# Kernel tuning notes

Hardware: AMD Instinct MI355X
Metric: run time of the kernel (lower is better)

Reference implementation:

```python
import jax, jax.numpy as jnp
import numpy as np

D_MODEL = 1024
D_INNER = 2048
D_STATE = 16
DT_RANK = 64
D_CONV = 4
EPS = 1e-5
B_SZ, L = 2, 2048


def setup_inputs() -> dict:
    key = jax.random.key(0)
    ks = jax.random.split(key, 8)
    s = 0.02
    inp = {
        "x": jax.random.normal(ks[0], (B_SZ, L, D_MODEL), jnp.float32),
        "in_proj_w": jax.random.normal(ks[1], (D_MODEL, 2 * D_INNER), jnp.float32) * s,
        "conv_w": jax.random.normal(ks[2], (D_INNER, 1, D_CONV), jnp.float32) * s,
        "conv_b": jnp.zeros((D_INNER,), jnp.float32),
        "x_proj_w": jax.random.normal(ks[3], (D_INNER, DT_RANK + 2 * D_STATE), jnp.float32) * s,
        "dt_proj_w": jax.random.normal(ks[4], (DT_RANK, D_INNER), jnp.float32) * s,
        "dt_proj_b": jax.random.normal(ks[5], (D_INNER,), jnp.float32) * s,
        "A_log": jnp.log(jnp.broadcast_to(jnp.arange(1, D_STATE + 1, dtype=jnp.float32), (D_INNER, D_STATE))),
        "D": jnp.ones((D_INNER,), jnp.float32),
        "out_proj_w": jax.random.normal(ks[6], (D_INNER, D_MODEL), jnp.float32) * s,
        "norm_w": jnp.ones((D_MODEL,), jnp.float32),
    }
    return inp


def _silu(x):
    return x * jax.nn.sigmoid(x)


def reference(x, in_proj_w, conv_w, conv_b, x_proj_w, dt_proj_w, dt_proj_b,
              A_log, D, out_proj_w, norm_w):
    b, l, d = x.shape
    # RMSNorm
    xn = x * jax.lax.rsqrt(jnp.mean(x * x, axis=-1, keepdims=True) + EPS) * norm_w
    # in_proj -> split into x branch and residual (gate) branch
    x_and_res = xn @ in_proj_w                      # (b, l, 2*d_inner)
    xi, res = jnp.split(x_and_res, 2, axis=-1)
    # causal depthwise conv1d (pad left d_conv-1, equivalent to torch pad+truncate)
    xc = jax.lax.conv_general_dilated(
        xi.transpose(0, 2, 1),                      # (b, d_inner, l)
        conv_w,                                     # (d_inner, 1, d_conv) = OIH
        window_strides=(1,),
        padding=[(D_CONV - 1, 0)],
        feature_group_count=D_INNER,
        dimension_numbers=("NCH", "OIH", "NCH"),
    ) + conv_b[None, :, None]
    xi = _silu(xc.transpose(0, 2, 1))               # (b, l, d_inner)
    # SSM parameters
    x_dbl = xi @ x_proj_w                           # (b, l, dt_rank + 2n)
    delta, Bm, Cm = jnp.split(x_dbl, [DT_RANK, DT_RANK + D_STATE], axis=-1)
    delta = jax.nn.softplus(delta @ dt_proj_w + dt_proj_b)   # (b, l, d_inner)
    A = -jnp.exp(A_log)                             # (d_inner, n)
    # discretize
    deltaA = jnp.exp(delta[..., None] * A)                          # (b,l,d,n)
    deltaB_u = delta[..., None] * Bm[:, :, None, :] * xi[..., None]  # (b,l,d,n)
    # selective scan over sequence length via lax.scan
    def step(state, inputs):
        dA_t, dBu_t, C_t = inputs                   # (b,d,n),(b,d,n),(b,n)
        state = dA_t * state + dBu_t
        y_t = jnp.einsum("bdn,bn->bd", state, C_t)
        return state, y_t
    state0 = jnp.zeros((b, D_INNER, D_STATE), xi.dtype)
    _, ys = jax.lax.scan(
        step, state0,
        (deltaA.transpose(1, 0, 2, 3), deltaB_u.transpose(1, 0, 2, 3), Cm.transpose(1, 0, 2)),
    )                                               # ys: (l, b, d_inner)
    y = ys.transpose(1, 0, 2) + xi * D              # skip connection D*u
    y = y * _silu(res)                              # gate
    out = y @ out_proj_w + x                        # out_proj + residual add
    return out
```

## Files before the change

kernel.cpp:

```cpp
#include <hip/hip_runtime.h>
#include <cstdint>

#define D_MODEL 1024
#define D_INNER 2048
#define NSTATE  16
#define DT_RANK 64
#define SEQ     2048
#define NBATCH  2
#define NTOK    (NBATCH * SEQ)

#define NC      32
#define CHK     64
#define NGRP    8

typedef float  f32x4  __attribute__((ext_vector_type(4)));
typedef __bf16 bf16x8 __attribute__((ext_vector_type(8)));
typedef short  s16x8  __attribute__((ext_vector_type(8)));

__device__ __forceinline__ unsigned short f2bf(float f) {
  union { float f; uint32_t u; } a; a.f = f;
  uint32_t u = a.u;
  uint32_t r = (u + 0x7FFFu + ((u >> 16) & 1u)) >> 16;
  return (unsigned short)r;
}
__device__ __forceinline__ float bf2f(unsigned short h) {
  union { uint32_t u; float f; } a; a.u = ((uint32_t)h) << 16;
  return a.f;
}

__device__ __forceinline__ void gload16(const void* g, void* l) {
  __builtin_amdgcn_global_load_lds((__attribute__((address_space(1))) void*)g,
                                   (__attribute__((address_space(3))) void*)l,
                                   16, 0, 0);
}

__device__ __forceinline__ void rms_body(const float* __restrict__ x, const float* __restrict__ nw,
                                         unsigned short* __restrict__ xn, int row, float* red) {
  const float4 v = ((const float4*)(x + (size_t)row * D_MODEL))[threadIdx.x];
  float ss = v.x*v.x + v.y*v.y + v.z*v.z + v.w*v.w;
  #pragma unroll
  for (int m = 32; m; m >>= 1) ss += __shfl_xor(ss, m);
  if ((threadIdx.x & 63) == 0) red[threadIdx.x >> 6] = ss;
  __syncthreads();
  const float tot = red[0] + red[1] + red[2] + red[3];
  const float rs = rsqrtf(tot * (1.0f / D_MODEL) + 1e-5f);
  const float4 w = ((const float4*)nw)[threadIdx.x];
  ushort4 o;
  o.x = f2bf(v.x * rs * w.x);
  o.y = f2bf(v.y * rs * w.y);
  o.z = f2bf(v.z * rs * w.z);
  o.w = f2bf(v.w * rs * w.w);
  ((ushort4*)(xn + (size_t)row * D_MODEL))[threadIdx.x] = o;
}

__device__ __forceinline__ void tr_body(const float* __restrict__ W, unsigned short* __restrict__ Wt,
                                        int K, int N, int Npad, int bx, int by, float (*tile)[33]) {
  const int tx = threadIdx.x & 31, ty = threadIdx.x >> 5;
  const int kt = by * 32, nt = bx * 32;
  #pragma unroll
  for (int i = 0; i < 4; ++i) {
    const int k = kt + ty + i*8, n = nt + tx;
    tile[ty + i*8][tx] = (k < K && n < N) ? W[(size_t)k * N + n] : 0.0f;
  }
  __syncthreads();
  #pragma unroll
  for (int i = 0; i < 4; ++i) {
    const int n = nt + ty + i*8, k = kt + tx;
    if (n < Npad && k < K) Wt[(size_t)n * K + k] = f2bf(tile[tx][ty + i*8]);
  }
}

__global__ __launch_bounds__(256) void prep_fused_kernel(const float* x, const float* nw, unsigned short* xn,
                                                         const float* W1, unsigned short* W1t,
                                                         const float* W2, unsigned short* W2t,
                                                         const float* W3, unsigned short* W3t,
                                                         const float* W4, unsigned short* W4t) {
  __shared__ float shbuf[32][33];
  const int b = blockIdx.x;
  if (b < 4096) {
    rms_body(x, nw, xn, b, &shbuf[0][0]);
  } else if (b < 8192) {
    const int i = b - 4096;
    tr_body(W1, W1t, 1024, 4096, 4096, i & 127, i >> 7, shbuf);
  } else if (b < 8448) {
    const int i = b - 8192;
    tr_body(W2, W2t, 2048, 96, 128, i & 3, i >> 2, shbuf);
  } else if (b < 8576) {
    const int i = b - 8448;
    tr_body(W3, W3t, 64, 2048, 2048, i & 63, i >> 6, shbuf);
  } else {
    const int i = b - 8576;
    tr_body(W4, W4t, 2048, 1024, 1024, i & 31, i >> 5, shbuf);
  }
}

__global__ __launch_bounds__(512, 2) void g0_inproj_kernel(const unsigned short* __restrict__ A,
                                                           const unsigned short* __restrict__ Bt,
                                                           unsigned short* __restrict__ xiOut,
                                                           unsigned short* __restrict__ resOut) {
  constexpr int K  = 1024;
  constexpr int NT = K / 64;
  __shared__ __align__(16) unsigned short sA[2][256 * 64];
  __shared__ __align__(16) unsigned short sB[2][256 * 64];
  const int tid = threadIdx.x;
  const int wid = tid >> 6, lane = tid & 63;
  const int wm = wid >> 2, wn = wid & 3;
  const int lr = lane & 15, kq = lane >> 4;
  const int m0 = blockIdx.y * 256, n0 = blockIdx.x * 256;

  f32x4 acc[8][4] = {};

  const int srow = tid >> 3;
  const int scol = 8 * ((tid & 7) ^ ((tid >> 3) & 7));
  const unsigned short* gA = A  + (size_t)(m0 + srow) * K + scol;
  const unsigned short* gB = Bt + (size_t)(n0 + srow) * K + scol;

  const int xsw = (lr & 7) << 4;
  const int cofs0 = ((kq * 16) ^ xsw) >> 1;
  const int cofs1 = ((64 + kq * 16) ^ xsw) >> 1;
  const int aRow = (wm * 128 + lr) * 64;
  const int bRow = (wn * 64 + lr) * 64;

  auto stage2 = [&](int p, int kt, int q) {
    const int k0 = kt * 64;
    gload16(gA + (size_t)q * 64 * K + k0, (char*)sA[p] + q * 8192 + tid * 16);
    gload16(gB + (size_t)q * 64 * K + k0, (char*)sB[p] + q * 8192 + tid * 16);
  };

  #pragma unroll
  for (int q = 0; q < 4; ++q) stage2(0, 0, q);
  __syncthreads();

  int p = 0;
  for (int kt = 0; kt < NT; ++kt) {
    const unsigned short* SA = sA[p];
    const unsigned short* SB = sB[p];
    bf16x8 b[4][2];
    #pragma unroll
    for (int q = 0; q < 4; ++q) {
      bf16x8 a[2][2];
      #pragma unroll
      for (int mi = 0; mi < 2; ++mi) {
        a[mi][0] = __builtin_bit_cast(bf16x8, *(const s16x8*)(SA + aRow + (2*q + mi) * 1024 + cofs0));
        a[mi][1] = __builtin_bit_cast(bf16x8, *(const s16x8*)(SA + aRow + (2*q + mi) * 1024 + cofs1));
      }
      if (q == 0) {
        #pragma unroll
        for (int nf = 0; nf < 4; ++nf) {
          b[nf][0] = __builtin_bit_cast(bf16x8, *(const s16x8*)(SB + bRow + nf * 1024 + cofs0));
          b[nf][1] = __builtin_bit_cast(bf16x8, *(const s16x8*)(SB + bRow + nf * 1024 + cofs1));
        }
      }
      if (kt + 1 < NT) stage2(p ^ 1, kt + 1, q);
      __builtin_amdgcn_s_barrier();
      __builtin_amdgcn_s_setprio(1);
      #pragma unroll
      for (int ks = 0; ks < 2; ++ks)
        #pragma unroll
        for (int mi = 0; mi < 2; ++mi)
          #pragma unroll
          for (int nf = 0; nf < 4; ++nf)
            acc[2*q + mi][nf] = __builtin_amdgcn_mfma_f32_16x16x32_bf16(a[mi][ks], b[nf][ks], acc[2*q + mi][nf], 0, 0, 0);
      __builtin_amdgcn_s_setprio(0);
      __builtin_amdgcn_s_barrier();
    }
    __syncthreads();
    p ^= 1;
  }

  #pragma unroll
  for (int mf = 0; mf < 8; ++mf) {
    #pragma unroll
    for (int nf = 0; nf < 4; ++nf) {
      const int col = n0 + wn * 64 + nf * 16 + lr;
      unsigned short* dst = (col < D_INNER)
          ? xiOut + col
          : resOut + (col - D_INNER);
      #pragma unroll
      for (int r = 0; r < 4; ++r) {
        const int row = m0 + wm * 128 + mf * 16 + kq * 4 + r;
        dst[(size_t)row * D_INNER] = f2bf(acc[mf][nf][r]);
      }
    }
  }
}

template<int MODE>
__device__ __forceinline__ void gemm_body(const unsigned short* __restrict__ A,
                                          const unsigned short* __restrict__ Bt,
                                          const int M, const int N, const int K,
                                          void* __restrict__ out0,
                                          void* __restrict__ out1,
                                          const float* __restrict__ extra) {
  __shared__ __align__(16) unsigned short sA[2][128 * 32];
  __shared__ __align__(16) unsigned short sB[2][128 * 32];
  const int tid = threadIdx.x;
  const int w = tid >> 6, lane = tid & 63;
  const int m0 = blockIdx.y * 128, n0 = blockIdx.x * 128;
  const int wm = w >> 1, wn = w & 1;
  const int lr = lane & 15, kq = lane >> 4;

  f32x4 acc[4][4] = {};

  const int r0 = tid >> 2;
  const int qb = ((tid & 3) ^ (r0 & 3)) * 16;
  const char* pA0 = (const char*)A + ((size_t)(m0 + r0)      * K) * 2 + qb;
  const char* pA1 = (const char*)A + ((size_t)(m0 + r0 + 64) * K) * 2 + qb;
  const char* pB0 = (const char*)Bt + ((size_t)(n0 + r0)      * K) * 2 + qb;
  const char* pB1 = (const char*)Bt + ((size_t)(n0 + r0 + 64) * K) * 2 + qb;

  const int kqs = (kq ^ (lr & 3)) * 8;

  auto stage = [&](int p, int k0) {
    gload16(pA0 + (size_t)k0 * 2, (char*)sA[p] + w * 1024);
    gload16(pA1 + (size_t)k0 * 2, (char*)sA[p] + 4096 + w * 1024);
    gload16(pB0 + (size_t)k0 * 2, (char*)sB[p] + w * 1024);
    gload16(pB1 + (size_t)k0 * 2, (char*)sB[p] + 4096 + w * 1024);
  };
  auto compute = [&](int p) {
    const unsigned short* pa = sA[p] + (wm*64 + lr) * 32 + kqs;
    const unsigned short* pb = sB[p] + (wn*64 + lr) * 32 + kqs;
    bf16x8 af[4], bb[4];
    #pragma unroll
    for (int mf = 0; mf < 4; ++mf)
      af[mf] = __builtin_bit_cast(bf16x8, *(const s16x8*)(pa + mf * 16 * 32));
    #pragma unroll
    for (int nf = 0; nf < 4; ++nf)
      bb[nf] = __builtin_bit_cast(bf16x8, *(const s16x8*)(pb + nf * 16 * 32));
    #pragma unroll
    for (int mf = 0; mf < 4; ++mf)
      #pragma unroll
      for (int nf = 0; nf < 4; ++nf)
        acc[mf][nf] = __builtin_amdgcn_mfma_f32_16x16x32_bf16(af[mf], bb[nf], acc[mf][nf], 0, 0, 0);
  };

  stage(0, 0);
  __syncthreads();
  int p = 0;
  for (int k0 = 32; k0 < K; k0 += 32) {
    stage(p ^ 1, k0);
    compute(p);
    __syncthreads();
    p ^= 1;
  }
  compute(p);

  #pragma unroll
  for (int mf = 0; mf < 4; ++mf) {
    #pragma unroll
    for (int nf = 0; nf < 4; ++nf) {
      #pragma unroll
      for (int r = 0; r < 4; ++r) {
        const int row = m0 + wm*64 + mf*16 + kq*4 + r;
        const int col = n0 + wn*64 + nf*16 + lr;
        const float v = acc[mf][nf][r];
        if constexpr (MODE == 1) {
          if (col < DT_RANK) ((unsigned short*)out0)[(size_t)row * DT_RANK + col] = f2bf(v);
          else if (col < DT_RANK + 2*NSTATE) ((float*)out1)[(size_t)row * (2*NSTATE) + (col - DT_RANK)] = v;
        } else if constexpr (MODE == 2) {
          const float t = v + extra[col];
          const float sp = (t > 30.0f) ? t : __logf(1.0f + __expf(t));
          ((unsigned short*)out0)[(size_t)row * D_INNER + col] = f2bf(sp);
        } else {
          ((float*)out0)[(size_t)row * D_MODEL + col] = v + extra[(size_t)row * D_MODEL + col];
        }
      }
    }
  }
}

__global__ __launch_bounds__(256) void g1_xproj_kernel(const unsigned short* A, const unsigned short* Bt,
                                                       int M, int N, int K, void* o0, void* o1, const float* ex) {
  gemm_body<1>(A, Bt, M, N, K, o0, o1, ex);
}
__global__ __launch_bounds__(256) void g2_dtproj_kernel(const unsigned short* A, const unsigned short* Bt,
                                                        int M, int N, int K, void* o0, void* o1, const float* ex) {
  gemm_body<2>(A, Bt, M, N, K, o0, o1, ex);
}
__global__ __launch_bounds__(256) void g3_outproj_kernel(const unsigned short* A, const unsigned short* Bt,
                                                         int M, int N, int K, void* o0, void* o1, const float* ex) {
  gemm_body<3>(A, Bt, M, N, K, o0, o1, ex);
}

__global__ __launch_bounds__(256) void conv_silu_kernel(const unsigned short* __restrict__ xi_raw,
                                                        const float* __restrict__ cw,
                                                        const float* __restrict__ cb,
                                                        unsigned short* __restrict__ xi) {
  const int t = blockIdx.x * 256 + threadIdx.x;
  const int d8 = (t & 255) * 8;
  const int row = t >> 8;
  const int l = row & (SEQ - 1);

  float acc[8];
  #pragma unroll
  for (int c = 0; c < 8; c += 4) {
    const f32x4 bv = *(const f32x4*)(cb + d8 + c);
    acc[c+0] = bv[0]; acc[c+1] = bv[1]; acc[c+2] = bv[2]; acc[c+3] = bv[3];
  }
  f32x4 wv[8];
  #pragma unroll
  for (int c = 0; c < 8; ++c) wv[c] = ((const f32x4*)cw)[d8 + c];

  #pragma unroll
  for (int tap = 0; tap < 4; ++tap) {
    const int lp = l - 3 + tap;
    if (lp >= 0) {
      const s16x8 v = *(const s16x8*)(xi_raw + (size_t)(row - 3 + tap) * D_INNER + d8);
      #pragma unroll
      for (int c = 0; c < 8; ++c)
        acc[c] += wv[c][tap] * bf2f((unsigned short)v[c]);
    }
  }
  s16x8 o;
  #pragma unroll
  for (int c = 0; c < 8; ++c) {
    const float a = acc[c] / (1.0f + __expf(-acc[c]));
    o[c] = (short)f2bf(a);
  }
  *(s16x8*)(xi + (size_t)row * D_INNER + d8) = o;
}

template<int PASS>
__global__ __launch_bounds__(256) void scan_pass_kernel(const unsigned short* __restrict__ delta,
                                                        const unsigned short* __restrict__ xi,
                                                        const unsigned short* __restrict__ res,
                                                        const float* __restrict__ BC,
                                                        const float* __restrict__ A_log,
                                                        const float* __restrict__ Dv,
                                                        const float* __restrict__ initS,
                                                        float* __restrict__ aprodOut,
                                                        float* __restrict__ sendOut,
                                                        unsigned short* __restrict__ yg) {
  const int tid = threadIdx.x;
  const int db = blockIdx.x & 7;
  const int c  = (blockIdx.x >> 3) & (NC - 1);
  const int b  = blockIdx.x >> 8;
  const int d  = db * 256 + tid;
  const int row0 = b * SEQ + c * CHK;
  const size_t ob = ((size_t)(b * NC + c) * D_INNER + d) * 16;

  float Ac[16];
  #pragma unroll
  for (int q = 0; q < 4; ++q) {
    f32x4 t = ((const f32x4*)(A_log + (size_t)d * 16))[q];
    Ac[q*4+0] = -expf(t[0]); Ac[q*4+1] = -expf(t[1]);
    Ac[q*4+2] = -expf(t[2]); Ac[q*4+3] = -expf(t[3]);
  }
  float s[16];
  float ap[16];
  if constexpr (PASS == 0) {
    #pragma unroll
    for (int n = 0; n < 16; ++n) { s[n] = 0.0f; ap[n] = 1.0f; }
  } else {
    #pragma unroll
    for (int q = 0; q < 4; ++q)
      ((f32x4*)s)[q] = ((const f32x4*)(initS + ob))[q];
  }
  float Dd = 0.0f;
  if constexpr (PASS == 1) Dd = Dv[d];

  __shared__ float bcbuf[2][8][32];
  auto stageg = [&](int g, int p) {
    bcbuf[p][tid >> 5][tid & 31] = BC[(size_t)(row0 + g * 8) * 32 + tid];
  };
  stageg(0, 0);

  for (int g = 0; g < NGRP; ++g) {
    unsigned short dl[8], uu[8], rr[8];
    #pragma unroll
    for (int j = 0; j < 8; ++j) {
      const size_t row = (size_t)(row0 + g * 8 + j) * D_INNER + d;
      dl[j] = delta[row];
      uu[j] = xi[row];
      if constexpr (PASS == 1) rr[j] = res[row];
    }
    __syncthreads();
    if (g + 1 < NGRP) stageg(g + 1, (g + 1) & 1);

    #pragma unroll
    for (int j = 0; j < 8; ++j) {
      const float dlt = bf2f(dl[j]);
      const float u   = bf2f(uu[j]);
      const float dlu = dlt * u;
      float bc[32];
      #pragma unroll
      for (int q = 0; q < (PASS ? 8 : 4); ++q)
        ((f32x4*)bc)[q] = ((const f32x4*)(&bcbuf[g & 1][j][0]))[q];
      #pragma unroll
      for (int n = 0; n < 16; ++n) {
        const float dA = __expf(dlt * Ac[n]);
        s[n] = dA * s[n] + dlu * bc[n];
        if constexpr (PASS == 0) ap[n] *= dA;
      }
      if constexpr (PASS == 1) {
        float y = 0.0f;
        #pragma unroll
        for (int n = 0; n < 16; ++n) y += s[n] * bc[16 + n];
        const float r = bf2f(rr[j]);
        const float o = (y + u * Dd) * (r / (1.0f + __expf(-r)));
        yg[(size_t)(row0 + g * 8 + j) * D_INNER + d] = f2bf(o);
      }
    }
  }

  if constexpr (PASS == 0) {
    #pragma unroll
    for (int q = 0; q < 4; ++q) {
      ((f32x4*)(aprodOut + ob))[q] = ((f32x4*)ap)[q];
      ((f32x4*)(sendOut + ob))[q]  = ((f32x4*)s)[q];
    }
  }
}

__global__ __launch_bounds__(256) void scan_combine_kernel(const float* __restrict__ aprod,
                                                           const float* __restrict__ send,
                                                           float* __restrict__ initS) {
  const int t = blockIdx.x * 256 + threadIdx.x;
  const int b = t >> 13;
  const int rq = t & 8191;
  f32x4 carry = {0.0f, 0.0f, 0.0f, 0.0f};
  #pragma unroll
  for (int c = 0; c < NC; ++c) {
    const size_t idx = (size_t)(b * NC + c) * 8192 + rq;
    ((f32x4*)initS)[idx] = carry;
    const f32x4 a = ((const f32x4*)aprod)[idx];
    const f32x4 e = ((const f32x4*)send)[idx];
    carry = a * carry + e;
  }
}

extern "C" void kernel_launch(void* const* d_in, const int* in_sizes, int n_in,
                              void* d_out, int out_size, void* d_ws, size_t ws_size,
                              hipStream_t stream) {
  const float* x        = (const float*)d_in[0];
  const float* in_proj  = (const float*)d_in[1];
  const float* conv_w   = (const float*)d_in[2];
  const float* conv_b   = (const float*)d_in[3];
  const float* x_proj   = (const float*)d_in[4];
  const float* dt_proj  = (const float*)d_in[5];
  const float* dt_b     = (const float*)d_in[6];
  const float* A_log    = (const float*)d_in[7];
  const float* Dv       = (const float*)d_in[8];
  const float* out_proj = (const float*)d_in[9];
  const float* norm_w   = (const float*)d_in[10];

  char* ws = (char*)d_ws;
  size_t off = 0;
  auto alloc = [&](size_t bytes) {
    char* p = ws + off; off += (bytes + 255) & ~(size_t)255; return p;
  };
  unsigned short* xn     = (unsigned short*)alloc((size_t)NTOK * D_MODEL * 2);
  unsigned short* W1t    = (unsigned short*)alloc((size_t)(2 * D_INNER) * D_MODEL * 2);
  unsigned short* xi_raw = (unsigned short*)alloc((size_t)NTOK * D_INNER * 2);
  unsigned short* resb   = (unsigned short*)alloc((size_t)NTOK * D_INNER * 2);
  unsigned short* xi     = (unsigned short*)alloc((size_t)NTOK * D_INNER * 2);
  unsigned short* W2t    = (unsigned short*)alloc((size_t)128 * D_INNER * 2);
  unsigned short* dr     = (unsigned short*)alloc((size_t)NTOK * DT_RANK * 2);
  float*          BC     = (float*)alloc((size_t)NTOK * 32 * 4);
  unsigned short* W3t    = (unsigned short*)alloc((size_t)D_INNER * DT_RANK * 2);
  unsigned short* dlt    = (unsigned short*)alloc((size_t)NTOK * D_INNER * 2);
  unsigned short* ygb    = (unsigned short*)alloc((size_t)NTOK * D_INNER * 2);
  unsigned short* W4t    = (unsigned short*)alloc((size_t)D_MODEL * D_INNER * 2);

  float* aprod = (float*)xi_raw;
  float* send  = (float*)((char*)xi_raw + 8388608);
  float* initS = (float*)xn;

  prep_fused_kernel<<<10624, 256, 0, stream>>>(x, norm_w, xn,
                                               in_proj, W1t, x_proj, W2t,
                                               dt_proj, W3t, out_proj, W4t);

  g0_inproj_kernel<<<dim3(4096/256, 4096/256), 512, 0, stream>>>(xn, W1t, xi_raw, resb);
  conv_silu_kernel<<<NTOK, 256, 0, stream>>>(xi_raw, conv_w, conv_b, xi);
  g1_xproj_kernel<<<dim3(1, 4096/128), 256, 0, stream>>>(xi, W2t, NTOK, 128, 2048, dr, BC, nullptr);
  g2_dtproj_kernel<<<dim3(2048/128, 4096/128), 256, 0, stream>>>(dr, W3t, NTOK, 2048, 64, dlt, nullptr, dt_b);

  scan_pass_kernel<0><<<NBATCH * NC * (D_INNER/256), 256, 0, stream>>>(
      dlt, xi, nullptr, BC, A_log, nullptr, nullptr, aprod, send, nullptr);
  scan_combine_kernel<<<64, 256, 0, stream>>>(aprod, send, initS);
  scan_pass_kernel<1><<<NBATCH * NC * (D_INNER/256), 256, 0, stream>>>(
      dlt, xi, resb, BC, A_log, Dv, initS, nullptr, nullptr, ygb);

  g3_outproj_kernel<<<dim3(1024/128, 4096/128), 256, 0, stream>>>(ygb, W4t, NTOK, 1024, 2048, d_out, nullptr, x);
}
```

Measured before the change: 350.3 us.

## Double GEMM K-tile to 64 with XOR-swizzled LDS and grouped block remap

Raises the K step of the shared bf16 MFMA GEMM body from 32 to 64. This halves the number of barriers and loop iterations and issues twice as many MFMAs per sync. The LDS layout becomes 128-byte rows with an 8-way XOR swizzle so fragment reads avoid bank conflicts. It also remaps block IDs to group tiles for better L2 locality. LDS use doubles to 64KB per block, which may reduce occupancy, and the remap assumes the grid size divides evenly by 8.

Result: faster. 331.2 us (-5.5%).

```diff
diff --git a/kernel.cpp b/kernel.cpp
--- a/kernel.cpp
+++ b/kernel.cpp
@@ -192,52 +192,64 @@
                                           void* __restrict__ out0,
                                           void* __restrict__ out1,
                                           const float* __restrict__ extra) {
-  __shared__ __align__(16) unsigned short sA[2][128 * 32];
-  __shared__ __align__(16) unsigned short sB[2][128 * 32];
+  __shared__ __align__(16) unsigned short sA[2][128 * 64];
+  __shared__ __align__(16) unsigned short sB[2][128 * 64];
   const int tid = threadIdx.x;
   const int w = tid >> 6, lane = tid & 63;
-  const int m0 = blockIdx.y * 128, n0 = blockIdx.x * 128;
+  const int nwg = gridDim.x * gridDim.y;
+  const int id  = blockIdx.x + gridDim.x * blockIdx.y;
+  const int swz = (id & 7) * (nwg >> 3) + (id >> 3);
+  const int bx = swz % gridDim.x, by = swz / gridDim.x;
+  const int m0 = by * 128, n0 = bx * 128;
   const int wm = w >> 1, wn = w & 1;
   const int lr = lane & 15, kq = lane >> 4;
 
   f32x4 acc[4][4] = {};
 
-  const int r0 = tid >> 2;
-  const int qb = ((tid & 3) ^ (r0 & 3)) * 16;
-  const char* pA0 = (const char*)A + ((size_t)(m0 + r0)      * K) * 2 + qb;
-  const char* pA1 = (const char*)A + ((size_t)(m0 + r0 + 64) * K) * 2 + qb;
-  const char* pB0 = (const char*)Bt + ((size_t)(n0 + r0)      * K) * 2 + qb;
-  const char* pB1 = (const char*)Bt + ((size_t)(n0 + r0 + 64) * K) * 2 + qb;
-
-  const int kqs = (kq ^ (lr & 3)) * 8;
+  const int srow = tid >> 3;
+  const int scol = 8 * ((tid & 7) ^ (srow & 7));
+  const unsigned short* gA = A  + (size_t)(m0 + srow) * K + scol;
+  const unsigned short* gB = Bt + (size_t)(n0 + srow) * K + scol;
 
   auto stage = [&](int p, int k0) {
-    gload16(pA0 + (size_t)k0 * 2, (char*)sA[p] + w * 1024);
-    gload16(pA1 + (size_t)k0 * 2, (char*)sA[p] + 4096 + w * 1024);
-    gload16(pB0 + (size_t)k0 * 2, (char*)sB[p] + w * 1024);
-    gload16(pB1 + (size_t)k0 * 2, (char*)sB[p] + 4096 + w * 1024);
+    #pragma unroll
+    for (int i = 0; i < 4; ++i) {
+      gload16(gA + (size_t)(32 * i) * K + k0, (char*)sA[p] + i * 4096 + tid * 16);
+      gload16(gB + (size_t)(32 * i) * K + k0, (char*)sB[p] + i * 4096 + tid * 16);
+    }
   };
+
+  const int xsw = (lr & 7) << 4;
+  const int c0 = ((kq * 16) ^ xsw) >> 1;
+  const int c1 = ((64 + kq * 16) ^ xsw) >> 1;
+
   auto compute = [&](int p) {
-    const unsigned short* pa = sA[p] + (wm*64 + lr) * 32 + kqs;
-    const unsigned short* pb = sB[p] + (wn*64 + lr) * 32 + kqs;
-    bf16x8 af[4], bb[4];
-    #pragma unroll
-    for (int mf = 0; mf < 4; ++mf)
-      af[mf] = __builtin_bit_cast(bf16x8, *(const s16x8*)(pa + mf * 16 * 32));
-    #pragma unroll
-    for (int nf = 0; nf < 4; ++nf)
-      bb[nf] = __builtin_bit_cast(bf16x8, *(const s16x8*)(pb + nf * 16 * 32));
-    #pragma unroll
-    for (int mf = 0; mf < 4; ++mf)
-      #pragma unroll
-      for (int nf = 0; nf < 4; ++nf)
-        acc[mf][nf] = __builtin_amdgcn_mfma_f32_16x16x32_bf16(af[mf], bb[nf], acc[mf][nf], 0, 0, 0);
+    const unsigned short* pa = sA[p] + (size_t)(wm * 64 + lr) * 64;
+    const unsigned short* pb = sB[p] + (size_t)(wn * 64 + lr) * 64;
+    bf16x8 af[4][2], bb[4][2];
+    #pragma unroll
+    for (int mf = 0; mf < 4; ++mf) {
+      af[mf][0] = __builtin_bit_cast(bf16x8, *(const s16x8*)(pa + mf * 16 * 64 + c0));
+      af[mf][1] = __builtin_bit_cast(bf16x8, *(const s16x8*)(pa + mf * 16 * 64 + c1));
+    }
+    #pragma unroll
+    for (int nf = 0; nf < 4; ++nf) {
+      bb[nf][0] = __builtin_bit_cast(bf16x8, *(const s16x8*)(pb + nf * 16 * 64 + c0));
+      bb[nf][1] = __builtin_bit_cast(bf16x8, *(const s16x8*)(pb + nf * 16 * 64 + c1));
+    }
+    #pragma unroll
+    for (int ks = 0; ks < 2; ++ks)
+      #pragma unroll
+      for (int mf = 0; mf < 4; ++mf)
+        #pragma unroll
+        for (int nf = 0; nf < 4; ++nf)
+          acc[mf][nf] = __builtin_amdgcn_mfma_f32_16x16x32_bf16(af[mf][ks], bb[nf][ks], acc[mf][nf], 0, 0, 0);
   };
 
   stage(0, 0);
   __syncthreads();
   int p = 0;
-  for (int k0 = 32; k0 < K; k0 += 32) {
+  for (int k0 = 64; k0 < K; k0 += 64) {
     stage(p ^ 1, k0);
     compute(p);
     __syncthreads();
```
